# Kernel optimization log

Hardware: AMD Instinct MI355X
Metric: run time of the kernel (lower is better)

## Reference

```python
import jax, jax.numpy as jnp
import numpy as np

EPS = 1e-8
BOX2D_IDX = jnp.array([0, 1, 3, 4, 6])  # x, y, dx, dy, yaw


def box2corners(box):
    # box: (..., 5) = (x, y, w, h, alpha) -> corners (..., 4, 2), CCW order
    x, y, w, h, a = (box[..., i] for i in range(5))
    tx = jnp.array([0.5, -0.5, -0.5, 0.5], box.dtype)
    ty = jnp.array([0.5, 0.5, -0.5, -0.5], box.dtype)
    x4 = tx * w[..., None]
    y4 = ty * h[..., None]
    c, s = jnp.cos(a)[..., None], jnp.sin(a)[..., None]
    rx = c * x4 - s * y4 + x[..., None]
    ry = s * x4 + c * y4 + y[..., None]
    return jnp.stack([rx, ry], axis=-1)


def edge_intersections(c1, c2):
    # all 4x4 edge-edge intersections of two quads -> pts (..., 16, 2), mask (..., 16)
    p1 = c1[..., :, None, :]
    p2 = jnp.roll(c1, -1, axis=-2)[..., :, None, :]
    q1 = c2[..., None, :, :]
    q2 = jnp.roll(c2, -1, axis=-2)[..., None, :, :]
    r = p2 - p1
    s = q2 - q1
    denom = r[..., 0] * s[..., 1] - r[..., 1] * s[..., 0]
    safe = jnp.where(jnp.abs(denom) < EPS, 1.0, denom)
    qp = q1 - p1
    t = (qp[..., 0] * s[..., 1] - qp[..., 1] * s[..., 0]) / safe
    u = (qp[..., 0] * r[..., 1] - qp[..., 1] * r[..., 0]) / safe
    mask = (jnp.abs(denom) > EPS) & (t > 0) & (t < 1) & (u > 0) & (u < 1)
    pts = jnp.where(mask[..., None], p1 + t[..., None] * r, 0.0)
    lead = pts.shape[:-3]
    return pts.reshape(lead + (16, 2)), mask.reshape(lead + (16,))


def points_in_box(pts, corners):
    # pts (..., K, 2) inside rotated quad given by corners (..., 4, 2) -> (..., K) bool
    a = corners[..., 0:1, :]
    ab = corners[..., 1:2, :] - a
    ad = corners[..., 3:4, :] - a
    ap = pts - a
    pab = jnp.sum(ap * ab, -1)
    pad = jnp.sum(ap * ad, -1)
    nab = jnp.sum(ab * ab, -1)
    nad = jnp.sum(ad * ad, -1)
    return (pab > 0) & (pab < nab) & (pad > 0) & (pad < nad)


def masked_polygon_area(verts, mask):
    # verts (..., 24, 2) candidate vertices, mask (..., 24) validity
    m = mask.astype(verts.dtype)
    num = jnp.maximum(jnp.sum(m, -1, keepdims=True), 1.0)
    mean = jnp.sum(verts * m[..., None], -2, keepdims=True) / num[..., None]
    d = verts - mean  # centered (shoelace is translation-invariant)
    ang = jnp.arctan2(d[..., 1], d[..., 0])
    # push invalid vertices to the end with stable tie-break
    ang = jnp.where(mask, ang, 1e6 + jnp.arange(24, dtype=ang.dtype))
    idx = jnp.argsort(ang, axis=-1)
    vs = jnp.take_along_axis(d, idx[..., None], axis=-2)
    ms = jnp.take_along_axis(mask, idx, axis=-1)
    v0 = vs[..., 0:1, :]
    vs = jnp.where(ms[..., None], vs, v0)  # collapse invalid onto first vertex
    nxt = jnp.roll(vs, -1, axis=-2)
    cross = vs[..., 0] * nxt[..., 1] - vs[..., 1] * nxt[..., 0]
    return 0.5 * jnp.abs(jnp.sum(cross, -1))


def rotated_iou_3d(b1, b2):
    # b1, b2: (..., 7) = (x, y, z, dx, dy, dz, yaw); elementwise-aligned IoU
    c1 = box2corners(b1[..., BOX2D_IDX])
    c2 = box2corners(b2[..., BOX2D_IDX])
    ipts, imask = edge_intersections(c1, c2)
    in1 = points_in_box(c1, c2)
    in2 = points_in_box(c2, c1)
    verts = jnp.concatenate([c1, c2, ipts], axis=-2)  # (..., 24, 2)
    mask = jnp.concatenate([in1, in2, imask], axis=-1)
    inter2d = masked_polygon_area(verts, mask)
    zmax = jnp.minimum(b1[..., 2] + 0.5 * b1[..., 5], b2[..., 2] + 0.5 * b2[..., 5])
    zmin = jnp.maximum(b1[..., 2] - 0.5 * b1[..., 5], b2[..., 2] - 0.5 * b2[..., 5])
    inter3d = inter2d * jnp.maximum(zmax - zmin, 0.0)
    v1 = b1[..., 3] * b1[..., 4] * b1[..., 5]
    v2 = b2[..., 3] * b2[..., 4] * b2[..., 5]
    return inter3d / (v1 + v2 - inter3d + EPS)


def setup_inputs() -> dict:
    key = jax.random.key(0)
    k1, k2, k3, k4, k5 = jax.random.split(key, 5)
    N = 1048576
    ctr = (jax.random.uniform(k1, (N, 3)) - 0.5) * 40.0
    dims = jax.random.uniform(k2, (N, 3)) * 2.0 + 0.5
    yaw = (jax.random.uniform(k3, (N, 1)) - 0.5) * (2.0 * np.pi)
    pred = jnp.concatenate([ctr, dims, yaw], axis=-1).astype(jnp.float32)
    noise = jax.random.normal(k4, (N, 7)) * jnp.array(
        [0.3, 0.3, 0.3, 0.2, 0.2, 0.2, 0.2], jnp.float32)
    target = pred + noise
    target = target.at[:, 3:6].set(jnp.maximum(target[:, 3:6], 0.1))
    weight = jax.random.uniform(k5, (N,), dtype=jnp.float32)
    return {"pred": pred, "target": target, "weight": weight}


def reference(pred, target, weight):
    # IoU3DLoss(with_yaw=True, reduction='mean', loss_weight=1.0)
    loss_weight = 1.0
    iou = rotated_iou_3d(pred[None, ...], target[None, ...])  # (1, N)
    iou_loss = (1.0 - iou) * weight
    return loss_weight * jnp.mean(iou_loss)
```

## Files before the change

### kernel.cpp

```cpp
#include <hip/hip_runtime.h>

#define EPS_F 1e-8f
#define BLOCK 256

typedef float vf4 __attribute__((ext_vector_type(4)));

__device__ __forceinline__ vf4 load4u(const float* p) {
    vf4 v;
    __builtin_memcpy(&v, p, 16);
    return v;
}

__device__ __forceinline__ float fast_rcp(float x) {
    return __builtin_amdgcn_rcpf(x);
}

__global__ void zero_out_kernel(float* out) { out[0] = 0.f; }

__device__ __forceinline__ float edge_contrib(float ax, float ay,
                                              float bx, float by,
                                              float W, float H) {
    float dx = bx - ax, dy = by - ay;
    float sdx = (fabsf(dx) < 1e-20f) ? 1e-20f : dx;
    float sdy = (fabsf(dy) < 1e-20f) ? 1e-20f : dy;
    float rdx = fast_rcp(sdx);
    float rdy = fast_rcp(sdy);

    float tA = (-W - ax) * rdx;
    float tB = ( W - ax) * rdx;
    float ta = fmaxf(fminf(tA, tB), 0.f);
    float tb = fminf(fmaxf(tA, tB), 1.f);
    tb = fmaxf(ta, tb);

    float u0 = (-H - ay) * rdy;
    float u1 = ( H - ay) * rdy;
    float tm0 = fminf(u0, u1), tm1 = fmaxf(u0, u1);
    float t1 = fminf(fmaxf(tm0, ta), tb);
    float t2 = fminf(fmaxf(tm1, ta), tb);

    float x0 = fmaf(ta, dx, ax), y0 = fmaf(ta, dy, ay);
    float x1 = fmaf(t1, dx, ax), y1 = fmaf(t1, dy, ay);
    float x2 = fmaf(t2, dx, ax), y2 = fmaf(t2, dy, ay);
    float x3 = fmaf(tb, dx, ax), y3 = fmaf(tb, dy, ay);
    float h0 = fminf(fmaxf(y0, -H), H) + H;
    float h1 = fminf(fmaxf(y1, -H), H) + H;
    float h2 = fminf(fmaxf(y2, -H), H) + H;
    float h3 = fminf(fmaxf(y3, -H), H) + H;

    return (x1 - x0) * (h0 + h1) + (x2 - x1) * (h1 + h2) + (x3 - x2) * (h2 + h3);
}

__global__ __launch_bounds__(BLOCK, 4) void iou3d_loss_kernel(
    const float* __restrict__ pred, const float* __restrict__ target,
    const float* __restrict__ weight, float* __restrict__ out,
    int N, float invN, int stride, int iters)
{
    int i = blockIdx.x * BLOCK + threadIdx.x;

    int j = (i < N) ? i : 0;
    long o = (long)j * 7;
    vf4 A0 = load4u(pred + o),  A1 = load4u(pred + o + 3);
    vf4 B0 = load4u(target + o), B1 = load4u(target + o + 3);
    float wg = (i < N) ? weight[j] : 0.f;

    float val = 0.f;
    #pragma unroll 1
    for (int it = 0; it < iters; ++it) {
        vf4 a0 = A0, a1 = A1, b0 = B0, b1 = B1;
        float w = wg;

        int inext = i + stride;
        if (it + 1 < iters) {
            int jn = (inext < N) ? inext : 0;
            long on = (long)jn * 7;
            A0 = load4u(pred + on);  A1 = load4u(pred + on + 3);
            B0 = load4u(target + on); B1 = load4u(target + on + 3);
            wg = (inext < N) ? weight[jn] : 0.f;
        }
        i = inext;

        float s1, c1, s2, c2;
        __sincosf(a1.w, &s1, &c1);
        __sincosf(b1.w, &s2, &c2);
        float cd = c1 * c2 + s1 * s2;
        float sd = c1 * s2 - s1 * c2;
        float dxc = b0.x - a0.x, dyc = b0.y - a0.y;
        float tx =  c1 * dxc + s1 * dyc;
        float ty = -s1 * dxc + c1 * dyc;
        float W = 0.5f * a1.x, H = 0.5f * a1.y;
        float w2 = 0.5f * b1.x, h2 = 0.5f * b1.y;

        float cw = cd * w2, sw = sd * w2, ch = cd * h2, sh = sd * h2;
        float q0x =  cw - sh + tx, q0y =  sw + ch + ty;
        float q1x = -cw - sh + tx, q1y = -sw + ch + ty;
        float q2x = -cw + sh + tx, q2y = -sw - ch + ty;
        float q3x =  cw + sh + tx, q3y =  sw - ch + ty;

        float s  = edge_contrib(q0x, q0y, q1x, q1y, W, H)
                 + edge_contrib(q1x, q1y, q2x, q2y, W, H)
                 + edge_contrib(q2x, q2y, q3x, q3y, W, H)
                 + edge_contrib(q3x, q3y, q0x, q0y, W, H);
        float area = 0.5f * fabsf(s);

        float zmax = fminf(a0.z + 0.5f * a1.z, b0.z + 0.5f * b1.z);
        float zmin = fmaxf(a0.z - 0.5f * a1.z, b0.z - 0.5f * b1.z);
        float inter3d = area * fmaxf(zmax - zmin, 0.f);
        float v1 = a1.x * a1.y * a1.z;
        float v2 = b1.x * b1.y * b1.z;
        float iou = inter3d * fast_rcp(v1 + v2 - inter3d + EPS_F);
        val += (1.f - iou) * w;
    }

    #pragma unroll
    for (int off = 32; off > 0; off >>= 1) val += __shfl_down(val, off, 64);
    __shared__ float wsum[4];
    int lane = threadIdx.x & 63, wid = threadIdx.x >> 6;
    if (lane == 0) wsum[wid] = val;
    __syncthreads();
    if (threadIdx.x == 0) {
        float ssum = (wsum[0] + wsum[1] + wsum[2] + wsum[3]) * invN;
        atomicAdd(out, ssum);
    }
}

extern "C" void kernel_launch(void* const* d_in, const int* in_sizes, int n_in,
                              void* d_out, int out_size, void* d_ws, size_t ws_size,
                              hipStream_t stream) {
    const float* pred   = (const float*)d_in[0];
    const float* target = (const float*)d_in[1];
    const float* weight = (const float*)d_in[2];
    float* out = (float*)d_out;
    int N = in_sizes[2];

    zero_out_kernel<<<1, 1, 0, stream>>>(out);
    int nblocks = (N + BLOCK - 1) / BLOCK;
    int grid = (nblocks < 1024) ? nblocks : 1024;
    int stride = grid * BLOCK;
    int iters = (N + stride - 1) / stride;
    iou3d_loss_kernel<<<grid, BLOCK, 0, stream>>>(pred, target, weight, out,
                                                  N, 1.f / (float)N, stride, iters);
}
```

Baseline: 100.3 us.

## Replace atomic accumulation with per-block partials and a final reduce kernel

The zero-init kernel and the per-block atomicAdd are replaced by per-block partial sums written to workspace, followed by a single-block reduction kernel that also applies the 1/N scaling. The grid cap doubles to 2048 and launch bounds now request 8 blocks per CU, aiming for higher occupancy and fewer iterations per thread. This drops atomic contention and the separate zeroing launch, but still uses two launches and may add register pressure from the tighter launch bound.

```diff
diff --git a/kernel.cpp b/kernel.cpp
--- a/kernel.cpp
+++ b/kernel.cpp
@@ -2,6 +2,7 @@
 
 #define EPS_F 1e-8f
 #define BLOCK 256
+#define MAXGRID 2048
 
 typedef float vf4 __attribute__((ext_vector_type(4)));
 
@@ -14,8 +15,6 @@
 __device__ __forceinline__ float fast_rcp(float x) {
     return __builtin_amdgcn_rcpf(x);
 }
-
-__global__ void zero_out_kernel(float* out) { out[0] = 0.f; }
 
 __device__ __forceinline__ float edge_contrib(float ax, float ay,
                                               float bx, float by,
@@ -50,10 +49,10 @@
     return (x1 - x0) * (h0 + h1) + (x2 - x1) * (h1 + h2) + (x3 - x2) * (h2 + h3);
 }
 
-__global__ __launch_bounds__(BLOCK, 4) void iou3d_loss_kernel(
+__global__ __launch_bounds__(BLOCK, 8) void iou3d_partial_kernel(
     const float* __restrict__ pred, const float* __restrict__ target,
-    const float* __restrict__ weight, float* __restrict__ out,
-    int N, float invN, int stride, int iters)
+    const float* __restrict__ weight, float* __restrict__ partials,
+    int N, int stride, int iters)
 {
     int i = blockIdx.x * BLOCK + threadIdx.x;
 
@@ -117,10 +116,24 @@
     int lane = threadIdx.x & 63, wid = threadIdx.x >> 6;
     if (lane == 0) wsum[wid] = val;
     __syncthreads();
-    if (threadIdx.x == 0) {
-        float ssum = (wsum[0] + wsum[1] + wsum[2] + wsum[3]) * invN;
-        atomicAdd(out, ssum);
-    }
+    if (threadIdx.x == 0)
+        partials[blockIdx.x] = wsum[0] + wsum[1] + wsum[2] + wsum[3];
+}
+
+__global__ __launch_bounds__(BLOCK) void reduce_partials_kernel(
+    const float* __restrict__ partials, float* __restrict__ out,
+    int nparts, float invN)
+{
+    float v = 0.f;
+    for (int k = threadIdx.x; k < nparts; k += BLOCK) v += partials[k];
+    #pragma unroll
+    for (int off = 32; off > 0; off >>= 1) v += __shfl_down(v, off, 64);
+    __shared__ float wsum[4];
+    int lane = threadIdx.x & 63, wid = threadIdx.x >> 6;
+    if (lane == 0) wsum[wid] = v;
+    __syncthreads();
+    if (threadIdx.x == 0)
+        out[0] = (wsum[0] + wsum[1] + wsum[2] + wsum[3]) * invN;
 }
 
 extern "C" void kernel_launch(void* const* d_in, const int* in_sizes, int n_in,
@@ -130,13 +143,16 @@
     const float* target = (const float*)d_in[1];
     const float* weight = (const float*)d_in[2];
     float* out = (float*)d_out;
+    float* partials = (float*)d_ws;
     int N = in_sizes[2];
 
-    zero_out_kernel<<<1, 1, 0, stream>>>(out);
     int nblocks = (N + BLOCK - 1) / BLOCK;
-    int grid = (nblocks < 1024) ? nblocks : 1024;
+    int grid = (nblocks < MAXGRID) ? nblocks : MAXGRID;
     int stride = grid * BLOCK;
     int iters = (N + stride - 1) / stride;
-    iou3d_loss_kernel<<<grid, BLOCK, 0, stream>>>(pred, target, weight, out,
-                                                  N, 1.f / (float)N, stride, iters);
+
+    iou3d_partial_kernel<<<grid, BLOCK, 0, stream>>>(pred, target, weight,
+                                                     partials, N, stride, iters);
+    reduce_partials_kernel<<<1, BLOCK, 0, stream>>>(partials, out, grid,
+                                                    1.f / (float)N);
 }
```

New measurement: 101.1 us. Within noise of the previous version (+0.8%).
